# Kernel optimization log

Measured on AMD Instinct MI355X. Metric: run time of the kernel, lower is better.

The kernel has to match this reference:

```python
import jax, jax.numpy as jnp
import numpy as np

RADIUS = 400.0
FIELD = 8000.0  # um extent of slide coordinate field


def setup_inputs() -> dict:
    key = jax.random.key(0)
    ks = jax.random.split(key, 8)
    B, N, D, H, K = 4, 4096, 1536, 512, 8
    images = jax.random.normal(ks[0], (B, N, D), dtype=jnp.float32)
    positions = jax.random.uniform(ks[1], (B, N, 2), dtype=jnp.float32) * FIELD
    W_feat = jax.random.normal(ks[2], (D, H), dtype=jnp.float32) * (1.0 / np.sqrt(D))
    b_feat = jnp.zeros((H,), dtype=jnp.float32)
    W_pos = jax.random.normal(ks[3], (2, H), dtype=jnp.float32) * 0.5
    W_gnn = jax.random.normal(ks[4], (H, H), dtype=jnp.float32) * (1.0 / np.sqrt(H))
    W_self = jax.random.normal(ks[5], (H, H), dtype=jnp.float32) * (1.0 / np.sqrt(H))
    anchors = jax.random.normal(ks[6], (K, D), dtype=jnp.float32)
    return {"images": images, "positions": positions, "W_feat": W_feat,
            "b_feat": b_feat, "W_pos": W_pos, "W_gnn": W_gnn,
            "W_self": W_self, "anchors": anchors}


def _radius_adjacency(pos):
    # pos: (N, 2). Dense O(N^2) radius graph (mirrors torch.cdist + mask).
    sq = jnp.sum(pos * pos, axis=-1)                       # (N,)
    d2 = sq[:, None] + sq[None, :] - 2.0 * (pos @ pos.T)   # (N, N)
    mask = d2 < (RADIUS * RADIUS)
    N = pos.shape[0]
    mask = mask & ~jnp.eye(N, dtype=bool)                  # no self-loops
    return mask.astype(pos.dtype)


def reference(images, positions, W_feat, b_feat, W_pos, W_gnn, W_self, anchors):
    # --- Stream A: explicit concept quantifier (cosine sim to anchors) ---
    x_norm = images / jnp.clip(jnp.linalg.norm(images, axis=-1, keepdims=True), 1e-12)
    a_norm = anchors / jnp.clip(jnp.linalg.norm(anchors, axis=-1, keepdims=True), 1e-12)
    scores = jnp.einsum('bnd,kd->bnk', x_norm, a_norm)     # (B, N, K)
    concept_profile = scores.mean(axis=1)                  # (B, K)

    # --- Stream B: feature extraction with positional encoding ---
    feat = images @ W_feat + b_feat + positions @ W_pos    # (B, N, H)

    # --- radius graph + one mean-aggregation GNN layer, per slide ---
    def per_graph(f, p):
        A = _radius_adjacency(p)                           # (N, N)
        deg = jnp.clip(A.sum(axis=-1, keepdims=True), 1.0) # (N, 1)
        h = jax.nn.relu(f)
        agg = (A @ h) / deg                                # mean over neighbors
        return jax.nn.relu(agg @ W_gnn + f @ W_self)       # (N, H)

    refined = jax.vmap(per_graph)(feat, positions)         # (B, N, H)
    latent_spatial = refined.mean(axis=1)                  # (B, H)  per-graph mean pool

    return jnp.concatenate([latent_spatial, concept_profile], axis=1)  # (B, H+K)
```

## Files before the change

kernel.cpp:

```cpp
#include <hip/hip_runtime.h>

#define B_ 4
#define N_ 4096
#define D_ 1536
#define H_ 512
#define K_ 8
#define M_ (B_*N_)
#define R2_ 160000.0f
#define CAP 192

typedef __attribute__((ext_vector_type(8))) short bf16x8;
typedef __attribute__((ext_vector_type(4))) float f32x4;
typedef __attribute__((ext_vector_type(2))) float f32x2;

__device__ __forceinline__ unsigned short f2bf(float f) {
  union { float f; unsigned u; } v; v.f = f;
  unsigned r = (v.u + 0x7FFFu + ((v.u >> 16) & 1u)) >> 16;
  return (unsigned short)r;
}

typedef const __attribute__((address_space(1))) unsigned int gas_u32;
typedef __attribute__((address_space(3))) unsigned int las_u32;
__device__ __forceinline__ void gl_lds16(const unsigned short* g, unsigned short* l) {
  __builtin_amdgcn_global_load_lds((gas_u32*)g, (las_u32*)l, 16, 0, 0);
}

__global__ __launch_bounds__(256) void k_prep(
    const float* __restrict__ Wf, const float* __restrict__ Wg, const float* __restrict__ Ws,
    const float* __restrict__ anchors, unsigned short* __restrict__ WfT,
    unsigned short* __restrict__ WgsT, float* __restrict__ anorm) {
  __shared__ float t[64][65];
  __shared__ float red[4];
  int bx = blockIdx.x, by = blockIdx.y, tid = threadIdx.x;
  if (by == 40) {
    int k = bx;
    float s = 0.f;
    for (int i = tid; i < D_; i += 256) { float v = anchors[k*D_ + i]; s += v*v; }
    #pragma unroll
    for (int off = 32; off; off >>= 1) s += __shfl_down(s, off);
    if ((tid & 63) == 0) red[tid >> 6] = s;
    __syncthreads();
    if (tid == 0) anorm[k] = fmaxf(sqrtf(red[0]+red[1]+red[2]+red[3]), 1e-12f);
    return;
  }
  const float* W; unsigned short* WT; int kt, outStride, outOff;
  if (by < 24)      { W = Wf; WT = WfT;  kt = by;      outStride = D_;   outOff = 0; }
  else if (by < 32) { W = Wg; WT = WgsT; kt = by - 24; outStride = 1024; outOff = 0; }
  else              { W = Ws; WT = WgsT; kt = by - 32; outStride = 1024; outOff = 512; }
  int tx = tid & 63, ty = tid >> 6;
  #pragma unroll
  for (int r = 0; r < 64; r += 4)
    t[ty + r][tx] = W[(size_t)(kt*64 + ty + r)*H_ + bx*64 + tx];
  __syncthreads();
  #pragma unroll
  for (int r = 0; r < 64; r += 4) {
    int n = bx*64 + ty + r;
    WT[(size_t)n*outStride + outOff + kt*64 + tx] = f2bf(t[tx][ty + r]);
  }
}

__global__ __launch_bounds__(256) void k_concept_cast(
    const float* __restrict__ images, const float* __restrict__ anchors,
    const float* __restrict__ anorm, unsigned short* __restrict__ imgs_bf,
    float* __restrict__ out) {
  __shared__ unsigned short sAb[K_*D_];
  __shared__ float sc[4][K_];
  int tid = threadIdx.x, lane = tid & 63, w = tid >> 6;
  {
    const float4* a4 = (const float4*)anchors;
    #pragma unroll
    for (int i = 0; i < 12; i++) {
      float4 a = a4[tid + 256*i];
      ushort4 s; s.x = f2bf(a.x); s.y = f2bf(a.y); s.z = f2bf(a.z); s.w = f2bf(a.w);
      ((ushort4*)sAb)[tid + 256*i] = s;
    }
  }
  __syncthreads();
  float acc_k[K_] = {};
  for (int r = 0; r < 4; r++) {
    int gm = blockIdx.x*16 + w*4 + r;
    const float4* xrow = (const float4*)(images + (size_t)gm*D_);
    float nrm = 0.f; float dot[K_] = {};
    #pragma unroll
    for (int it = 0; it < 6; it++) {
      int j = lane + 64*it;
      float4 x = xrow[j];
      nrm += x.x*x.x + x.y*x.y + x.z*x.z + x.w*x.w;
      #pragma unroll
      for (int k = 0; k < K_; k++) {
        uint2 a = *(const uint2*)&sAb[k*D_ + j*4];
        union { unsigned u; float f; } c;
        float s = 0.f;
        c.u = a.x << 16;         s += x.x*c.f;
        c.u = a.x & 0xFFFF0000u; s += x.y*c.f;
        c.u = a.y << 16;         s += x.z*c.f;
        c.u = a.y & 0xFFFF0000u; s += x.w*c.f;
        dot[k] += s;
      }
      ushort4 s;
      s.x = f2bf(x.x); s.y = f2bf(x.y); s.z = f2bf(x.z); s.w = f2bf(x.w);
      *(ushort4*)&imgs_bf[(size_t)gm*D_ + (size_t)j*4] = s;
    }
    #pragma unroll
    for (int off = 32; off; off >>= 1) {
      nrm += __shfl_down(nrm, off);
      #pragma unroll
      for (int k = 0; k < K_; k++) dot[k] += __shfl_down(dot[k], off);
    }
    if (lane == 0) {
      float inv = 1.0f / fmaxf(sqrtf(nrm), 1e-12f);
      #pragma unroll
      for (int k = 0; k < K_; k++) acc_k[k] += dot[k] * inv / anorm[k];
    }
  }
  if (lane == 0) {
    #pragma unroll
    for (int k = 0; k < K_; k++) sc[w][k] = acc_k[k];
  }
  __syncthreads();
  if (tid < K_) {
    float s = sc[0][tid] + sc[1][tid] + sc[2][tid] + sc[3][tid];
    int b = blockIdx.x >> 8;
    atomicAdd(out + b*(H_+K_) + H_ + tid, s * (1.0f/N_));
  }
}

#define BM 128
#define BN 128
#define BK 32

__global__ __launch_bounds__(256) void k_gemm(
    const unsigned short* __restrict__ A, const unsigned short* __restrict__ BT,
    int Kdim, int mode, const float* __restrict__ bias, const float* __restrict__ Wpos,
    const float* __restrict__ positions, unsigned short* __restrict__ AB,
    unsigned char* __restrict__ P, float* __restrict__ out) {
  __shared__ __align__(16) unsigned short As[BM*BK];
  __shared__ unsigned short Bs[BN*BK];
  __shared__ float colsum[BN];
  int tid = threadIdx.x;
  int lane = tid & 63, wv = tid >> 6;
  int wm = wv >> 1, wn = wv & 1;
  int l15 = lane & 15, quad = lane >> 4;
  int bx = blockIdx.x;
  int bm = bx >> 2, bn = bx & 3;
  int m0 = bm*BM, n0 = bn*BN;

  f32x4 acc[4][4] = {};

  int c = wv*2;
  int rowc = (lane >> 2), seg = lane & 3;
  const unsigned short* gA0 = A  + (size_t)(m0 + c*16 + rowc)*Kdim + seg*8;
  const unsigned short* gA1 = gA0 + (size_t)16*Kdim;
  const unsigned short* gB0 = BT + (size_t)(n0 + c*16 + rowc)*Kdim + seg*8;
  const unsigned short* gB1 = gB0 + (size_t)16*Kdim;
  unsigned short* lA0 = As + c*512;
  unsigned short* lA1 = lA0 + 512;
  unsigned short* lB0 = Bs + c*512;
  unsigned short* lB1 = lB0 + 512;

  int nk = Kdim / BK;
  for (int kt = 0; kt < nk; kt++) {
    __syncthreads();
    gl_lds16(gA0, lA0); gl_lds16(gA1, lA1);
    gl_lds16(gB0, lB0); gl_lds16(gB1, lB1);
    gA0 += BK; gA1 += BK; gB0 += BK; gB1 += BK;
    __syncthreads();

    bf16x8 aF[4], bF[4];
    #pragma unroll
    for (int f = 0; f < 4; f++)
      aF[f] = *(const bf16x8*)&As[(wm*64 + f*16 + l15)*BK + quad*8];
    #pragma unroll
    for (int f = 0; f < 4; f++)
      bF[f] = *(const bf16x8*)&Bs[(wn*64 + f*16 + l15)*BK + quad*8];
    #pragma unroll
    for (int mi = 0; mi < 4; mi++)
      #pragma unroll
      for (int ni = 0; ni < 4; ni++)
        acc[mi][ni] = __builtin_amdgcn_mfma_f32_16x16x32_bf16(aF[mi], bF[ni], acc[mi][ni], 0, 0, 0);
  }

  if (mode == 0) {
    float bz[4], w0v[4], w1v[4];
    #pragma unroll
    for (int ni = 0; ni < 4; ni++) {
      int gh = n0 + wn*64 + ni*16 + l15;
      bz[ni] = bias[gh]; w0v[ni] = Wpos[gh]; w1v[ni] = Wpos[H_ + gh];
    }
    __syncthreads();
    float* sb = ((float*)As) + wv*256;
    int col4 = n0 + wn*64 + l15*4;
    #pragma unroll
    for (int mi = 0; mi < 4; mi++) {
      #pragma unroll
      for (int r = 0; r < 4; r++) {
        int gm = m0 + wm*64 + mi*16 + quad*4 + r;
        float2 p = ((const float2*)positions)[gm];
        #pragma unroll
        for (int ni = 0; ni < 4; ni++) {
          float v = acc[mi][ni][r] + bz[ni] + p.x*w0v[ni] + p.y*w1v[ni];
          sb[quad*64 + ni*16 + l15] = v;
        }
        f32x4 q = *(f32x4*)&sb[quad*64 + l15*4];
        uint2 o;
        o.x = ((unsigned)f2bf(q[1]) << 16) | f2bf(q[0]);
        o.y = ((unsigned)f2bf(q[3]) << 16) | f2bf(q[2]);
        *(uint2*)&AB[(size_t)gm*1024 + 512 + col4] = o;
        float e0 = fminf(fmaxf(q[0], 0.f)*0.015625f, 448.f);
        float e1 = fminf(fmaxf(q[1], 0.f)*0.015625f, 448.f);
        float e2 = fminf(fmaxf(q[2], 0.f)*0.015625f, 448.f);
        float e3 = fminf(fmaxf(q[3], 0.f)*0.015625f, 448.f);
        int u = __builtin_amdgcn_cvt_pk_fp8_f32(e0, e1, 0, false);
        u     = __builtin_amdgcn_cvt_pk_fp8_f32(e2, e3, u, true);
        *(unsigned*)(P + (size_t)gm*512 + col4) = (unsigned)u;
      }
    }
  } else {
    if (tid < BN) colsum[tid] = 0.f;
    __syncthreads();
    #pragma unroll
    for (int ni = 0; ni < 4; ni++) {
      float s = 0.f;
      #pragma unroll
      for (int mi = 0; mi < 4; mi++) {
        #pragma unroll
        for (int r = 0; r < 4; r++) s += fmaxf(acc[mi][ni][r], 0.f);
      }
      s += __shfl_down(s, 32);
      s += __shfl_down(s, 16);
      if (quad == 0) atomicAdd(&colsum[wn*64 + ni*16 + l15], s);
    }
    __syncthreads();
    if (tid < BN) {
      int b = m0 >> 12;
      atomicAdd(out + b*(H_+K_) + n0 + tid, colsum[tid] * (1.0f/N_));
    }
  }
}

__device__ __forceinline__ void accf8(uint2 v, float* a) {
  f32x2 p;
  p = __builtin_amdgcn_cvt_pk_f32_fp8(v.x, false); a[0] += p[0]; a[1] += p[1];
  p = __builtin_amdgcn_cvt_pk_f32_fp8(v.x, true);  a[2] += p[0]; a[3] += p[1];
  p = __builtin_amdgcn_cvt_pk_f32_fp8(v.y, false); a[4] += p[0]; a[5] += p[1];
  p = __builtin_amdgcn_cvt_pk_f32_fp8(v.y, true);  a[6] += p[0]; a[7] += p[1];
}

__global__ __launch_bounds__(256) void k_aggregate(const float* __restrict__ positions,
                                                   const unsigned char* __restrict__ P,
                                                   unsigned short* __restrict__ AB) {
  __shared__ unsigned short nl[8*CAP];
  __shared__ int cnt[8];
  __shared__ float sdx[8], sdy[8];
  int blk = blockIdx.x;
  int xcd = blk & 7;
  int b = xcd >> 1;
  int sub = ((blk >> 3) << 1) | (xcd & 1);
  int dest0 = sub * 8;
  int tid = threadIdx.x, lane = tid & 63, w = tid >> 6;
  const float2* p2 = (const float2*)(positions + (size_t)b*N_*2);
  if (tid < 8) {
    cnt[tid] = 0;
    float2 pd = p2[dest0 + tid];
    sdx[tid] = pd.x; sdy[tid] = pd.y;
  }
  __syncthreads();
  for (int it = 0; it < 16; it++) {
    int j = tid + 256*it;
    float2 pj = p2[j];
    #pragma unroll
    for (int d = 0; d < 8; d++) {
      float dx = pj.x - sdx[d], dy = pj.y - sdy[d];
      if (dx*dx + dy*dy < R2_ && j != dest0 + d) {
        int p = atomicAdd(&cnt[d], 1);
        if (p < CAP) nl[d*CAP + p] = (unsigned short)j;
      }
    }
  }
  __syncthreads();
  const unsigned char* featb = P + ((size_t)(b << 12))*512 + lane*8;
  #pragma unroll
  for (int dd = 0; dd < 2; dd++) {
    int d = w*2 + dd;
    int deg = cnt[d]; if (deg > CAP) deg = CAP;
    float inv = 64.0f / (float)(deg > 1 ? deg : 1);
    const unsigned short* nlp = &nl[d*CAP];
    float a[8] = {};
    int n = 0;
    for (; n + 4 <= deg; n += 4) {
      ushort4 idx = *(const ushort4*)&nlp[n];
      uint2 v0 = *(const uint2*)(featb + (size_t)idx.x*512);
      uint2 v1 = *(const uint2*)(featb + (size_t)idx.y*512);
      uint2 v2 = *(const uint2*)(featb + (size_t)idx.z*512);
      uint2 v3 = *(const uint2*)(featb + (size_t)idx.w*512);
      accf8(v0, a); accf8(v1, a); accf8(v2, a); accf8(v3, a);
    }
    for (; n < deg; n++) {
      int j = nlp[n];
      uint2 v = *(const uint2*)(featb + (size_t)j*512);
      accf8(v, a);
    }
    uint4 o;
    o.x = ((unsigned)f2bf(a[1]*inv) << 16) | f2bf(a[0]*inv);
    o.y = ((unsigned)f2bf(a[3]*inv) << 16) | f2bf(a[2]*inv);
    o.z = ((unsigned)f2bf(a[5]*inv) << 16) | f2bf(a[4]*inv);
    o.w = ((unsigned)f2bf(a[7]*inv) << 16) | f2bf(a[6]*inv);
    *(uint4*)(AB + (size_t)((b << 12) + dest0 + d)*1024 + lane*8) = o;
  }
}

extern "C" void kernel_launch(void* const* d_in, const int* in_sizes, int n_in,
                              void* d_out, int out_size, void* d_ws, size_t ws_size,
                              hipStream_t stream) {
  const float* images    = (const float*)d_in[0];
  const float* positions = (const float*)d_in[1];
  const float* W_feat    = (const float*)d_in[2];
  const float* b_feat    = (const float*)d_in[3];
  const float* W_pos     = (const float*)d_in[4];
  const float* W_gnn     = (const float*)d_in[5];
  const float* W_self    = (const float*)d_in[6];
  const float* anchors   = (const float*)d_in[7];
  float* out = (float*)d_out;

  char* ws = (char*)d_ws;
  unsigned short* imgs_bf = (unsigned short*)ws;
  unsigned short* AB      = (unsigned short*)(ws + 50331648);
  unsigned short* WfT     = (unsigned short*)(ws + 83886080);
  unsigned short* WgsT    = (unsigned short*)(ws + 85458944);
  unsigned char*  P       = (unsigned char*)(ws + 86507520);
  float*          anorm   = (float*)(ws + 94896128);

  hipMemsetAsync(d_out, 0, sizeof(float)*B_*(H_+K_), stream);
  k_prep<<<dim3(8, 41), 256, 0, stream>>>(W_feat, W_gnn, W_self, anchors, WfT, WgsT, anorm);
  k_concept_cast<<<M_/16, 256, 0, stream>>>(images, anchors, anorm, imgs_bf, out);
  k_gemm<<<512, 256, 0, stream>>>(imgs_bf, WfT, D_, 0, b_feat, W_pos, positions, AB, P, out);
  k_aggregate<<<2048, 256, 0, stream>>>(positions, P, AB);
  k_gemm<<<512, 256, 0, stream>>>(AB, WgsT, 1024, 1, nullptr, nullptr, nullptr, AB, nullptr, out);
}
```

Baseline: 286.3 us.

## Merge prep and cast kernels; compute concept scores via MFMA in GEMM

Folds the weight-transpose prep and the image cast into one launch, with the cast now storing only per-row inverse norms. The anchor dot products move out of scalar FMA code and into 128 extra blocks of the feature GEMM launch. Those blocks reread the bf16 images and run MFMA against zero-padded bf16 anchors. This removes one kernel launch and the heavy per-element scalar dot work in the cast, at the cost of reading the bf16 images a second time and using bf16 images instead of fp32 in the cosine scores.

```diff
diff --git a/kernel.cpp b/kernel.cpp
--- a/kernel.cpp
+++ b/kernel.cpp
@@ -25,104 +25,68 @@
   __builtin_amdgcn_global_load_lds((gas_u32*)g, (las_u32*)l, 16, 0, 0);
 }
 
-__global__ __launch_bounds__(256) void k_prep(
+#define CAST_BLKS 4096
+
+__global__ __launch_bounds__(256) void k_prepcast(
+    const float* __restrict__ images, const float* __restrict__ anchors,
     const float* __restrict__ Wf, const float* __restrict__ Wg, const float* __restrict__ Ws,
-    const float* __restrict__ anchors, unsigned short* __restrict__ WfT,
-    unsigned short* __restrict__ WgsT, float* __restrict__ anorm) {
-  __shared__ float t[64][65];
-  __shared__ float red[4];
-  int bx = blockIdx.x, by = blockIdx.y, tid = threadIdx.x;
-  if (by == 40) {
-    int k = bx;
+    unsigned short* __restrict__ imgs_bf, float* __restrict__ inv_norm,
+    unsigned short* __restrict__ WfT, unsigned short* __restrict__ WgsT,
+    unsigned short* __restrict__ ancT, float* __restrict__ invanorm) {
+  int tid = threadIdx.x;
+  if (blockIdx.x >= CAST_BLKS) {
+    int bi = blockIdx.x - CAST_BLKS;
+    if (bi < 320) {
+      __shared__ float t[64][65];
+      int bx = bi & 7, by = bi >> 3;
+      const float* W; unsigned short* WT; int kt, outStride, outOff;
+      if (by < 24)      { W = Wf; WT = WfT;  kt = by;      outStride = D_;   outOff = 0; }
+      else if (by < 32) { W = Wg; WT = WgsT; kt = by - 24; outStride = 1024; outOff = 0; }
+      else              { W = Ws; WT = WgsT; kt = by - 32; outStride = 1024; outOff = 512; }
+      int tx = tid & 63, ty = tid >> 6;
+      #pragma unroll
+      for (int r = 0; r < 64; r += 4)
+        t[ty + r][tx] = W[(size_t)(kt*64 + ty + r)*H_ + bx*64 + tx];
+      __syncthreads();
+      #pragma unroll
+      for (int r = 0; r < 64; r += 4) {
+        int n = bx*64 + ty + r;
+        WT[(size_t)n*outStride + outOff + kt*64 + tx] = f2bf(t[tx][ty + r]);
+      }
+      return;
+    }
+    __shared__ float red[4];
+    int k = bi - 320;
     float s = 0.f;
-    for (int i = tid; i < D_; i += 256) { float v = anchors[k*D_ + i]; s += v*v; }
+    for (int i = tid; i < D_; i += 256) {
+      float v = anchors[k*D_ + i];
+      s += v*v;
+      ancT[(size_t)k*D_ + i] = f2bf(v);
+      ancT[(size_t)(k+8)*D_ + i] = 0;
+    }
     #pragma unroll
     for (int off = 32; off; off >>= 1) s += __shfl_down(s, off);
     if ((tid & 63) == 0) red[tid >> 6] = s;
     __syncthreads();
-    if (tid == 0) anorm[k] = fmaxf(sqrtf(red[0]+red[1]+red[2]+red[3]), 1e-12f);
+    if (tid == 0) invanorm[k] = 1.0f / fmaxf(sqrtf(red[0]+red[1]+red[2]+red[3]), 1e-12f);
     return;
   }
-  const float* W; unsigned short* WT; int kt, outStride, outOff;
-  if (by < 24)      { W = Wf; WT = WfT;  kt = by;      outStride = D_;   outOff = 0; }
-  else if (by < 32) { W = Wg; WT = WgsT; kt = by - 24; outStride = 1024; outOff = 0; }
-  else              { W = Ws; WT = WgsT; kt = by - 32; outStride = 1024; outOff = 512; }
-  int tx = tid & 63, ty = tid >> 6;
+  int lane = tid & 63, w = tid >> 6;
+  int row = blockIdx.x*4 + w;
+  const float4* xr = (const float4*)(images + (size_t)row*D_);
+  ushort4* ob = (ushort4*)(imgs_bf + (size_t)row*D_);
+  float nrm = 0.f;
   #pragma unroll
-  for (int r = 0; r < 64; r += 4)
-    t[ty + r][tx] = W[(size_t)(kt*64 + ty + r)*H_ + bx*64 + tx];
-  __syncthreads();
+  for (int it = 0; it < 6; it++) {
+    float4 x = xr[lane + 64*it];
+    nrm += x.x*x.x + x.y*x.y + x.z*x.z + x.w*x.w;
+    ushort4 s;
+    s.x = f2bf(x.x); s.y = f2bf(x.y); s.z = f2bf(x.z); s.w = f2bf(x.w);
+    ob[lane + 64*it] = s;
+  }
   #pragma unroll
-  for (int r = 0; r < 64; r += 4) {
-    int n = bx*64 + ty + r;
-    WT[(size_t)n*outStride + outOff + kt*64 + tx] = f2bf(t[tx][ty + r]);
-  }
-}
-
-__global__ __launch_bounds__(256) void k_concept_cast(
-    const float* __restrict__ images, const float* __restrict__ anchors,
-    const float* __restrict__ anorm, unsigned short* __restrict__ imgs_bf,
-    float* __restrict__ out) {
-  __shared__ unsigned short sAb[K_*D_];
-  __shared__ float sc[4][K_];
-  int tid = threadIdx.x, lane = tid & 63, w = tid >> 6;
-  {
-    const float4* a4 = (const float4*)anchors;
-    #pragma unroll
-    for (int i = 0; i < 12; i++) {
-      float4 a = a4[tid + 256*i];
-      ushort4 s; s.x = f2bf(a.x); s.y = f2bf(a.y); s.z = f2bf(a.z); s.w = f2bf(a.w);
-      ((ushort4*)sAb)[tid + 256*i] = s;
-    }
-  }
-  __syncthreads();
-  float acc_k[K_] = {};
-  for (int r = 0; r < 4; r++) {
-    int gm = blockIdx.x*16 + w*4 + r;
-    const float4* xrow = (const float4*)(images + (size_t)gm*D_);
-    float nrm = 0.f; float dot[K_] = {};
-    #pragma unroll
-    for (int it = 0; it < 6; it++) {
-      int j = lane + 64*it;
-      float4 x = xrow[j];
-      nrm += x.x*x.x + x.y*x.y + x.z*x.z + x.w*x.w;
-      #pragma unroll
-      for (int k = 0; k < K_; k++) {
-        uint2 a = *(const uint2*)&sAb[k*D_ + j*4];
-        union { unsigned u; float f; } c;
-        float s = 0.f;
-        c.u = a.x << 16;         s += x.x*c.f;
-        c.u = a.x & 0xFFFF0000u; s += x.y*c.f;
-        c.u = a.y << 16;         s += x.z*c.f;
-        c.u = a.y & 0xFFFF0000u; s += x.w*c.f;
-        dot[k] += s;
-      }
-      ushort4 s;
-      s.x = f2bf(x.x); s.y = f2bf(x.y); s.z = f2bf(x.z); s.w = f2bf(x.w);
-      *(ushort4*)&imgs_bf[(size_t)gm*D_ + (size_t)j*4] = s;
-    }
-    #pragma unroll
-    for (int off = 32; off; off >>= 1) {
-      nrm += __shfl_down(nrm, off);
-      #pragma unroll
-      for (int k = 0; k < K_; k++) dot[k] += __shfl_down(dot[k], off);
-    }
-    if (lane == 0) {
-      float inv = 1.0f / fmaxf(sqrtf(nrm), 1e-12f);
-      #pragma unroll
-      for (int k = 0; k < K_; k++) acc_k[k] += dot[k] * inv / anorm[k];
-    }
-  }
-  if (lane == 0) {
-    #pragma unroll
-    for (int k = 0; k < K_; k++) sc[w][k] = acc_k[k];
-  }
-  __syncthreads();
-  if (tid < K_) {
-    float s = sc[0][tid] + sc[1][tid] + sc[2][tid] + sc[3][tid];
-    int b = blockIdx.x >> 8;
-    atomicAdd(out + b*(H_+K_) + H_ + tid, s * (1.0f/N_));
-  }
+  for (int off = 32; off; off >>= 1) nrm += __shfl_down(nrm, off);
+  if (lane == 0) inv_norm[row] = 1.0f / fmaxf(sqrtf(nrm), 1e-12f);
 }
 
 #define BM 128
@@ -133,15 +97,55 @@
     const unsigned short* __restrict__ A, const unsigned short* __restrict__ BT,
     int Kdim, int mode, const float* __restrict__ bias, const float* __restrict__ Wpos,
     const float* __restrict__ positions, unsigned short* __restrict__ AB,
-    unsigned char* __restrict__ P, float* __restrict__ out) {
+    unsigned char* __restrict__ P, const unsigned short* __restrict__ ancT,
+    const float* __restrict__ invnorm, const float* __restrict__ invanorm,
+    float* __restrict__ out) {
   __shared__ __align__(16) unsigned short As[BM*BK];
   __shared__ unsigned short Bs[BN*BK];
   __shared__ float colsum[BN];
   int tid = threadIdx.x;
   int lane = tid & 63, wv = tid >> 6;
-  int wm = wv >> 1, wn = wv & 1;
   int l15 = lane & 15, quad = lane >> 4;
   int bx = blockIdx.x;
+
+  if (mode == 0 && bx >= 512) {
+    int bm = bx - 512;
+    int m0 = bm*BM;
+    int c = wv*2, rowc = lane >> 2, seg = lane & 3;
+    const unsigned short* gA0 = A + (size_t)(m0 + c*16 + rowc)*Kdim + seg*8;
+    const unsigned short* gA1 = gA0 + (size_t)16*Kdim;
+    unsigned short* lA0 = As + c*512;
+    unsigned short* lA1 = lA0 + 512;
+    const unsigned short* anc = ancT + l15*D_ + quad*8;
+    f32x4 cacc[2] = {};
+    int nk = Kdim / BK;
+    for (int kt = 0; kt < nk; kt++) {
+      __syncthreads();
+      gl_lds16(gA0, lA0); gl_lds16(gA1, lA1);
+      gA0 += BK; gA1 += BK;
+      __syncthreads();
+      bf16x8 ancF = *(const bf16x8*)anc; anc += BK;
+      #pragma unroll
+      for (int f = 0; f < 2; f++) {
+        bf16x8 aF = *(const bf16x8*)&As[(wv*32 + f*16 + l15)*BK + quad*8];
+        cacc[f] = __builtin_amdgcn_mfma_f32_16x16x32_bf16(aF, ancF, cacc[f], 0, 0, 0);
+      }
+    }
+    float invA = (l15 < K_) ? invanorm[l15] : 0.f;
+    float part = 0.f;
+    #pragma unroll
+    for (int f = 0; f < 2; f++) {
+      float4 q = *(const float4*)&invnorm[m0 + wv*32 + f*16 + quad*4];
+      part += cacc[f][0]*q.x + cacc[f][1]*q.y + cacc[f][2]*q.z + cacc[f][3]*q.w;
+    }
+    part *= invA;
+    part += __shfl_down(part, 32);
+    part += __shfl_down(part, 16);
+    if (lane < K_) atomicAdd(out + (m0 >> 12)*(H_+K_) + H_ + lane, part * (1.0f/N_));
+    return;
+  }
+
+  int wm = wv >> 1, wn = wv & 1;
   int bm = bx >> 2, bn = bx & 3;
   int m0 = bm*BM, n0 = bn*BN;
 
@@ -328,12 +332,16 @@
   unsigned short* WfT     = (unsigned short*)(ws + 83886080);
   unsigned short* WgsT    = (unsigned short*)(ws + 85458944);
   unsigned char*  P       = (unsigned char*)(ws + 86507520);
-  float*          anorm   = (float*)(ws + 94896128);
+  float*          invanorm= (float*)(ws + 94896128);
+  unsigned short* ancT    = (unsigned short*)(ws + 94896160);
+  float*          inv_norm= (float*)(ws + 94945312);
 
   hipMemsetAsync(d_out, 0, sizeof(float)*B_*(H_+K_), stream);
-  k_prep<<<dim3(8, 41), 256, 0, stream>>>(W_feat, W_gnn, W_self, anchors, WfT, WgsT, anorm);
-  k_concept_cast<<<M_/16, 256, 0, stream>>>(images, anchors, anorm, imgs_bf, out);
-  k_gemm<<<512, 256, 0, stream>>>(imgs_bf, WfT, D_, 0, b_feat, W_pos, positions, AB, P, out);
+  k_prepcast<<<CAST_BLKS + 320 + 8, 256, 0, stream>>>(images, anchors, W_feat, W_gnn, W_self,
+                                                      imgs_bf, inv_norm, WfT, WgsT, ancT, invanorm);
+  k_gemm<<<640, 256, 0, stream>>>(imgs_bf, WfT, D_, 0, b_feat, W_pos, positions, AB, P,
+                                  ancT, inv_norm, invanorm, out);
   k_aggregate<<<2048, 256, 0, stream>>>(positions, P, AB);
-  k_gemm<<<512, 256, 0, stream>>>(AB, WgsT, 1024, 1, nullptr, nullptr, nullptr, AB, nullptr, out);
-}
+  k_gemm<<<512, 256, 0, stream>>>(AB, WgsT, 1024, 1, nullptr, nullptr, nullptr, AB, nullptr,
+                                  nullptr, nullptr, nullptr, out);
+}
```

After: 301.8 us. 1.05x slower.
